# Kernel optimization log

Measured on AMD Instinct MI355X. Metric: run time of the kernel, lower is better.

## Reference

```python
import jax, jax.numpy as jnp
import numpy as np


def setup_inputs() -> dict:
    key = jax.random.key(0)
    ks = jax.random.split(key, 7)
    B, T, D, H, DK, S = 16, 1, 4096, 32, 128, 2048
    return {
        "x": jax.random.normal(ks[0], (B, T, D), dtype=jnp.float32),
        "k_cache": jax.random.normal(ks[1], (B, H, S, DK), dtype=jnp.float32),
        "v_cache": jax.random.normal(ks[2], (B, H, S, DK), dtype=jnp.float32),
        "Wq": jax.random.normal(ks[3], (D, D), dtype=jnp.float32) * (D ** -0.5),
        "Wk": jax.random.normal(ks[4], (D, D), dtype=jnp.float32) * (D ** -0.5),
        "Wv": jax.random.normal(ks[5], (D, D), dtype=jnp.float32) * (D ** -0.5),
        "Wo": jax.random.normal(ks[6], (D, D), dtype=jnp.float32) * (D ** -0.5),
        "start_pos": 2047,
    }


def reference(x, k_cache, v_cache, Wq, Wk, Wv, Wo, start_pos):
    B, T, D = x.shape
    H, DK = k_cache.shape[1], k_cache.shape[3]
    end_pos = start_pos + T

    # QKV projections (nn.Linear with bias=False: y = x @ W.T), split heads -> (B, H, T, DK)
    def proj(W):
        return (x @ W.T).reshape(B, T, H, DK).transpose(0, 2, 1, 3)

    q = proj(Wq)
    k_new = proj(Wk)
    v_new = proj(Wv)

    # Scatter new K/V into the pre-allocated cache at start_pos (static slice)
    k_cache = jax.lax.dynamic_update_slice(k_cache, k_new, (0, 0, start_pos, 0))
    v_cache = jax.lax.dynamic_update_slice(v_cache, v_new, (0, 0, start_pos, 0))

    # Gather cached K/V up to end_pos
    k_all = k_cache[:, :, :end_pos]  # (B, H, end_pos, DK)
    v_all = v_cache[:, :, :end_pos]

    # Scaled dot-product attention with causal mask over cache positions
    scores = jnp.einsum("bhtd,bhsd->bhts", q, k_all) / jnp.sqrt(jnp.float32(DK))
    pos_q = start_pos + jnp.arange(T)          # query absolute positions
    pos_k = jnp.arange(end_pos)                # key absolute positions
    mask = pos_k[None, :] <= pos_q[:, None]    # (T, end_pos)
    scores = jnp.where(mask[None, None], scores, jnp.float32(-1e30))
    attn = jax.nn.softmax(scores, axis=-1)
    out = jnp.einsum("bhts,bhsd->bhtd", attn, v_all)

    # Merge heads and output projection
    out = out.transpose(0, 2, 1, 3).reshape(B, T, D)
    return out @ Wo.T
```

## Files before the change

### kernel.cpp

```cpp
#include <hip/hip_runtime.h>
#include <math.h>

constexpr int B  = 16;
constexpr int H  = 32;
constexpr int S  = 2048;
constexpr int DK = 128;
constexpr int D  = 4096;
constexpr int BH = B * H;

constexpr int NSPLIT = 4;
constexpr int CHUNK  = S / NSPLIT;
constexpr int NREC   = NSPLIT * 4;
constexpr int REC    = 132;

__device__ __forceinline__ float reduce64(float v[64], int lane) {
    #pragma unroll
    for (int s = 0; s < 6; ++s) {
        const int off = 1 << s;
        #pragma unroll
        for (int j = 0; j < (64 >> (s + 1)); ++j) {
            const float lo = v[2 * j], hi = v[2 * j + 1];
            const bool  up = (lane & off) != 0;
            const float mine = up ? hi : lo;
            const float oth  = up ? lo : hi;
            v[j] = mine + __shfl_xor(oth, off, 64);
        }
    }
    return v[0];
}

__global__ __launch_bounds__(256, 3) void proj_qkv_kernel(
    const float* __restrict__ X,
    const float* __restrict__ W0,
    const float* __restrict__ W1,
    const float* __restrict__ W2,
    float* __restrict__ Y0,
    float* __restrict__ Y1,
    float* __restrict__ Y2)
{
    __shared__ float4 xs[2][16][64];

    const int t    = threadIdx.x;
    const int lane = t & 63;
    const int wid  = t >> 6;
    const int tb   = t >> 4;
    const int tf   = t & 15;

    const int c0   = blockIdx.x * 16 + wid * 4;
    const int wsel = c0 >> 12;
    const int n0   = c0 & (D - 1);

    const float* Wp = (wsel == 0) ? W0 : (wsel == 1) ? W1 : W2;
    float*       Yp = (wsel == 0) ? Y0 : (wsel == 1) ? Y1 : Y2;
    const float4* w4 = (const float4*)Wp;
    const float4* x4 = (const float4*)X;

    float acc[64];
    #pragma unroll
    for (int i = 0; i < 64; ++i) acc[i] = 0.f;

    float4 xr[4];
    #pragma unroll
    for (int i = 0; i < 4; ++i) xr[i] = x4[tb * 1024 + tf + 16 * i];
    float4 wv[4];
    #pragma unroll
    for (int c = 0; c < 4; ++c) wv[c] = w4[(size_t)(n0 + c) * 1024 + lane];
    #pragma unroll
    for (int i = 0; i < 4; ++i) xs[0][tb][tf + 16 * i] = xr[i];
    __syncthreads();

    for (int ch = 0; ch < 16; ++ch) {
        float4 xn[4], wn[4];
        const bool more = (ch < 15);
        if (more) {
            #pragma unroll
            for (int i = 0; i < 4; ++i)
                xn[i] = x4[tb * 1024 + (ch + 1) * 64 + tf + 16 * i];
            #pragma unroll
            for (int c = 0; c < 4; ++c)
                wn[c] = w4[(size_t)(n0 + c) * 1024 + (ch + 1) * 64 + lane];
        }
        const int buf = ch & 1;
        #pragma unroll
        for (int b = 0; b < 16; ++b) {
            const float4 xv = xs[buf][b][lane];
            #pragma unroll
            for (int c = 0; c < 4; ++c)
                acc[b * 4 + c] += xv.x * wv[c].x + xv.y * wv[c].y +
                                  xv.z * wv[c].z + xv.w * wv[c].w;
        }
        if (more) {
            #pragma unroll
            for (int i = 0; i < 4; ++i) xs[buf ^ 1][tb][tf + 16 * i] = xn[i];
            __syncthreads();
            #pragma unroll
            for (int c = 0; c < 4; ++c) wv[c] = wn[c];
        }
    }

    const float outv = reduce64(acc, lane);
    Yp[(size_t)(lane >> 2) * D + n0 + (lane & 3)] = outv;
}

__global__ __launch_bounds__(256) void proj_wo_kernel(
    const float* __restrict__ X,
    const float* __restrict__ Wo,
    float* __restrict__ out)
{
    __shared__ float red[4][64];
    const int lane = threadIdx.x & 63;
    const int wid  = threadIdx.x >> 6;
    const int n0   = blockIdx.x * 4;
    const float4* w4 = (const float4*)Wo;
    const float4* x4 = (const float4*)X;

    float acc[64];
    #pragma unroll
    for (int i = 0; i < 64; ++i) acc[i] = 0.f;

    #pragma unroll
    for (int it = 0; it < 4; ++it) {
        const int d4 = wid * 256 + it * 64 + lane;
        float4 wv[4];
        #pragma unroll
        for (int c = 0; c < 4; ++c) wv[c] = w4[(size_t)(n0 + c) * 1024 + d4];
        #pragma unroll
        for (int b = 0; b < 16; ++b) {
            const float4 xv = x4[b * 1024 + d4];
            #pragma unroll
            for (int c = 0; c < 4; ++c)
                acc[b * 4 + c] += xv.x * wv[c].x + xv.y * wv[c].y +
                                  xv.z * wv[c].z + xv.w * wv[c].w;
        }
    }

    const float pv = reduce64(acc, lane);
    red[wid][lane] = pv;
    __syncthreads();
    if (wid == 0) {
        const float tot = red[0][lane] + red[1][lane] + red[2][lane] + red[3][lane];
        out[(size_t)(lane >> 2) * D + n0 + (lane & 3)] = tot;
    }
}

__global__ __launch_bounds__(256) void attn_kernel(
    const float* __restrict__ q,
    const float* __restrict__ k_cache,
    const float* __restrict__ v_cache,
    const float* __restrict__ k_new,
    const float* __restrict__ v_new,
    const int*   __restrict__ start_pos_p,
    float* __restrict__ part)
{
    const int lane  = threadIdx.x & 63;
    const int wid   = threadIdx.x >> 6;
    const int half  = lane >> 5;
    const int hl    = lane & 31;
    const int bh    = blockIdx.x & (BH - 1);
    const int split = blockIdx.x >> 9;

    const int sp    = start_pos_p[0];
    const int s0    = split * CHUNK;
    const int lim   = sp + 1;
    const int s_end = (s0 + CHUNK < lim) ? (s0 + CHUNK) : lim;

    const float qscale = 0.08838834764831845f * 1.4426950408889634f;
    const float shift  = 8.0f * 1.4426950408889634f;
    float4 qv = *(const float4*)(q + (size_t)bh * DK + 4 * hl);
    qv.x *= qscale; qv.y *= qscale; qv.z *= qscale; qv.w *= qscale;

    const float* kbase = k_cache + (size_t)bh * S * DK;
    const float* vbase = v_cache + (size_t)bh * S * DK;
    const float* knew  = k_new + (size_t)bh * DK;
    const float* vnew  = v_new + (size_t)bh * DK;

    float  l = 0.f;
    float4 acc = make_float4(0.f, 0.f, 0.f, 0.f);

    #pragma unroll 2
    for (int s2 = s0 + 2 * wid; s2 < s_end; s2 += 8) {
        const int  pos   = s2 + half;
        const bool valid = pos < s_end;
        const int  cpos  = valid ? pos : (s_end - 1);
        const float* kp = (cpos == sp) ? knew : (kbase + (size_t)cpos * DK);
        const float* vp = (cpos == sp) ? vnew : (vbase + (size_t)cpos * DK);
        const float4 kv = *(const float4*)(kp + 4 * hl);
        const float4 vv = *(const float4*)(vp + 4 * hl);

        float p = kv.x * qv.x + kv.y * qv.y + kv.z * qv.z + kv.w * qv.w;
        p += __shfl_xor(p, 1, 64);
        p += __shfl_xor(p, 2, 64);
        p += __shfl_xor(p, 4, 64);
        p += __shfl_xor(p, 8, 64);
        p += __shfl_xor(p, 16, 64);

        const float ep = valid ? __builtin_amdgcn_exp2f(p - shift) : 0.f;
        l     += ep;
        acc.x += ep * vv.x;
        acc.y += ep * vv.y;
        acc.z += ep * vv.z;
        acc.w += ep * vv.w;
    }

    l     += __shfl_xor(l, 32, 64);
    acc.x += __shfl_xor(acc.x, 32, 64);
    acc.y += __shfl_xor(acc.y, 32, 64);
    acc.z += __shfl_xor(acc.z, 32, 64);
    acc.w += __shfl_xor(acc.w, 32, 64);

    float* rec = part + ((size_t)bh * NREC + split * 4 + wid) * REC;
    if (half == 0) *(float4*)(rec + 4 * hl) = acc;
    if (lane == 0) rec[128] = l;
}

__global__ __launch_bounds__(64) void combine_kernel(
    const float* __restrict__ part,
    float* __restrict__ attn_out)
{
    const int bh   = blockIdx.x;
    const int lane = threadIdx.x;
    const float* base = part + (size_t)bh * NREC * REC;

    float L = 0.f, o0 = 0.f, o1 = 0.f;
    #pragma unroll
    for (int i = 0; i < NREC; ++i) {
        L += base[i * REC + 128];
        const float2 a = *(const float2*)(base + i * REC + 2 * lane);
        o0 += a.x;
        o1 += a.y;
    }
    const float inv = 1.f / L;
    attn_out[(size_t)bh * DK + 2 * lane]     = o0 * inv;
    attn_out[(size_t)bh * DK + 2 * lane + 1] = o1 * inv;
}

extern "C" void kernel_launch(void* const* d_in, const int* in_sizes, int n_in,
                              void* d_out, int out_size, void* d_ws, size_t ws_size,
                              hipStream_t stream)
{
    const float* x       = (const float*)d_in[0];
    const float* k_cache = (const float*)d_in[1];
    const float* v_cache = (const float*)d_in[2];
    const float* Wq      = (const float*)d_in[3];
    const float* Wk      = (const float*)d_in[4];
    const float* Wv      = (const float*)d_in[5];
    const float* Wo      = (const float*)d_in[6];
    const int*   sp      = (const int*)d_in[7];
    float*       out     = (float*)d_out;

    float* ws       = (float*)d_ws;
    float* q        = ws;
    float* k_new    = ws + 65536;
    float* v_new    = ws + 131072;
    float* attn_out = ws + 196608;
    float* part     = ws + 262144;

    proj_qkv_kernel<<<(3 * D) / 16, 256, 0, stream>>>(x, Wq, Wk, Wv, q, k_new, v_new);

    attn_kernel<<<BH * NSPLIT, 256, 0, stream>>>(q, k_cache, v_cache, k_new, v_new,
                                                 sp, part);

    combine_kernel<<<BH, 64, 0, stream>>>(part, attn_out);

    proj_wo_kernel<<<D / 4, 256, 0, stream>>>(attn_out, Wo, out);
}
```

Measured before the change: 307.0 us.

## Unify projection kernels into templated 2-column-per-wave GEMV with single LDS buffer

Replaces the QKV and Wo projection kernels with one templated kernel in which each wave computes 2 output columns instead of 4. The QKV launch uses 512-thread blocks and the Wo launch reuses the same staged-x path. This cuts register pressure (32 accumulators instead of 64) and raises the number of waves in flight for the bandwidth-bound weight streaming. The x tile in LDS drops from double to single buffering, which adds an extra barrier per chunk. The attention loop unroll also goes from 2 to 4.

```diff
diff --git a/kernel.cpp b/kernel.cpp
--- a/kernel.cpp
+++ b/kernel.cpp
@@ -13,12 +13,12 @@
 constexpr int NREC   = NSPLIT * 4;
 constexpr int REC    = 132;
 
-__device__ __forceinline__ float reduce64(float v[64], int lane) {
-    #pragma unroll
-    for (int s = 0; s < 6; ++s) {
+__device__ __forceinline__ float reduce32(float v[32], int lane) {
+    #pragma unroll
+    for (int s = 0; s < 5; ++s) {
         const int off = 1 << s;
         #pragma unroll
-        for (int j = 0; j < (64 >> (s + 1)); ++j) {
+        for (int j = 0; j < (32 >> (s + 1)); ++j) {
             const float lo = v[2 * j], hi = v[2 * j + 1];
             const bool  up = (lane & off) != 0;
             const float mine = up ? hi : lo;
@@ -26,10 +26,11 @@
             v[j] = mine + __shfl_xor(oth, off, 64);
         }
     }
-    return v[0];
-}
-
-__global__ __launch_bounds__(256, 3) void proj_qkv_kernel(
+    return v[0] + __shfl_xor(v[0], 32, 64);
+}
+
+template <int NT>
+__global__ __launch_bounds__(NT, 4) void proj_kernel(
     const float* __restrict__ X,
     const float* __restrict__ W0,
     const float* __restrict__ W1,
@@ -38,15 +39,19 @@
     float* __restrict__ Y1,
     float* __restrict__ Y2)
 {
-    __shared__ float4 xs[2][16][64];
+    constexpr int NW  = NT / 64;
+    constexpr int TPB = NT / 16;
+    constexpr int XPT = 64 / TPB;
+
+    __shared__ float4 xs[16][64];
 
     const int t    = threadIdx.x;
     const int lane = t & 63;
     const int wid  = t >> 6;
-    const int tb   = t >> 4;
-    const int tf   = t & 15;
-
-    const int c0   = blockIdx.x * 16 + wid * 4;
+    const int tb   = t / TPB;
+    const int tf   = t % TPB;
+
+    const int c0   = blockIdx.x * (NW * 2) + wid * 2;
     const int wsel = c0 >> 12;
     const int n0   = c0 & (D - 1);
 
@@ -55,92 +60,56 @@
     const float4* w4 = (const float4*)Wp;
     const float4* x4 = (const float4*)X;
 
-    float acc[64];
-    #pragma unroll
-    for (int i = 0; i < 64; ++i) acc[i] = 0.f;
-
-    float4 xr[4];
-    #pragma unroll
-    for (int i = 0; i < 4; ++i) xr[i] = x4[tb * 1024 + tf + 16 * i];
-    float4 wv[4];
-    #pragma unroll
-    for (int c = 0; c < 4; ++c) wv[c] = w4[(size_t)(n0 + c) * 1024 + lane];
-    #pragma unroll
-    for (int i = 0; i < 4; ++i) xs[0][tb][tf + 16 * i] = xr[i];
+    const size_t r0 = (size_t)(n0 + 0) * 1024;
+    const size_t r1 = (size_t)(n0 + 1) * 1024;
+
+    float acc[32];
+    #pragma unroll
+    for (int i = 0; i < 32; ++i) acc[i] = 0.f;
+
+    float4 xr[XPT];
+    #pragma unroll
+    for (int i = 0; i < XPT; ++i) xr[i] = x4[tb * 1024 + tf + TPB * i];
+    float4 wv0 = w4[r0 + lane];
+    float4 wv1 = w4[r1 + lane];
+    #pragma unroll
+    for (int i = 0; i < XPT; ++i) xs[tb][tf + TPB * i] = xr[i];
     __syncthreads();
 
     for (int ch = 0; ch < 16; ++ch) {
-        float4 xn[4], wn[4];
+        float4 xn[XPT], wn0, wn1;
         const bool more = (ch < 15);
         if (more) {
+            const int kb = (ch + 1) * 64;
             #pragma unroll
-            for (int i = 0; i < 4; ++i)
-                xn[i] = x4[tb * 1024 + (ch + 1) * 64 + tf + 16 * i];
-            #pragma unroll
-            for (int c = 0; c < 4; ++c)
-                wn[c] = w4[(size_t)(n0 + c) * 1024 + (ch + 1) * 64 + lane];
-        }
-        const int buf = ch & 1;
+            for (int i = 0; i < XPT; ++i)
+                xn[i] = x4[tb * 1024 + kb + tf + TPB * i];
+            wn0 = w4[r0 + kb + lane];
+            wn1 = w4[r1 + kb + lane];
+        }
+
         #pragma unroll
         for (int b = 0; b < 16; ++b) {
-            const float4 xv = xs[buf][b][lane];
-            #pragma unroll
-            for (int c = 0; c < 4; ++c)
-                acc[b * 4 + c] += xv.x * wv[c].x + xv.y * wv[c].y +
-                                  xv.z * wv[c].z + xv.w * wv[c].w;
-        }
+            const float4 xv = xs[b][lane];
+            acc[b * 2 + 0] += xv.x * wv0.x + xv.y * wv0.y +
+                              xv.z * wv0.z + xv.w * wv0.w;
+            acc[b * 2 + 1] += xv.x * wv1.x + xv.y * wv1.y +
+                              xv.z * wv1.z + xv.w * wv1.w;
+        }
+
         if (more) {
-            #pragma unroll
-            for (int i = 0; i < 4; ++i) xs[buf ^ 1][tb][tf + 16 * i] = xn[i];
             __syncthreads();
             #pragma unroll
-            for (int c = 0; c < 4; ++c) wv[c] = wn[c];
-        }
-    }
-
-    const float outv = reduce64(acc, lane);
-    Yp[(size_t)(lane >> 2) * D + n0 + (lane & 3)] = outv;
-}
-
-__global__ __launch_bounds__(256) void proj_wo_kernel(
-    const float* __restrict__ X,
-    const float* __restrict__ Wo,
-    float* __restrict__ out)
-{
-    __shared__ float red[4][64];
-    const int lane = threadIdx.x & 63;
-    const int wid  = threadIdx.x >> 6;
-    const int n0   = blockIdx.x * 4;
-    const float4* w4 = (const float4*)Wo;
-    const float4* x4 = (const float4*)X;
-
-    float acc[64];
-    #pragma unroll
-    for (int i = 0; i < 64; ++i) acc[i] = 0.f;
-
-    #pragma unroll
-    for (int it = 0; it < 4; ++it) {
-        const int d4 = wid * 256 + it * 64 + lane;
-        float4 wv[4];
-        #pragma unroll
-        for (int c = 0; c < 4; ++c) wv[c] = w4[(size_t)(n0 + c) * 1024 + d4];
-        #pragma unroll
-        for (int b = 0; b < 16; ++b) {
-            const float4 xv = x4[b * 1024 + d4];
-            #pragma unroll
-            for (int c = 0; c < 4; ++c)
-                acc[b * 4 + c] += xv.x * wv[c].x + xv.y * wv[c].y +
-                                  xv.z * wv[c].z + xv.w * wv[c].w;
-        }
-    }
-
-    const float pv = reduce64(acc, lane);
-    red[wid][lane] = pv;
-    __syncthreads();
-    if (wid == 0) {
-        const float tot = red[0][lane] + red[1][lane] + red[2][lane] + red[3][lane];
-        out[(size_t)(lane >> 2) * D + n0 + (lane & 3)] = tot;
-    }
+            for (int i = 0; i < XPT; ++i) xs[tb][tf + TPB * i] = xn[i];
+            __syncthreads();
+            wv0 = wn0;
+            wv1 = wn1;
+        }
+    }
+
+    const float tot = reduce32(acc, lane);
+    if (lane < 32)
+        Yp[(size_t)(lane >> 1) * D + n0 + (lane & 1)] = tot;
 }
 
 __global__ __launch_bounds__(256) void attn_kernel(
@@ -177,7 +146,7 @@
     float  l = 0.f;
     float4 acc = make_float4(0.f, 0.f, 0.f, 0.f);
 
-    #pragma unroll 2
+    #pragma unroll 4
     for (int s2 = s0 + 2 * wid; s2 < s_end; s2 += 8) {
         const int  pos   = s2 + half;
         const bool valid = pos < s_end;
@@ -255,12 +224,12 @@
     float* attn_out = ws + 196608;
     float* part     = ws + 262144;
 
-    proj_qkv_kernel<<<(3 * D) / 16, 256, 0, stream>>>(x, Wq, Wk, Wv, q, k_new, v_new);
+    proj_kernel<512><<<768, 512, 0, stream>>>(x, Wq, Wk, Wv, q, k_new, v_new);
 
     attn_kernel<<<BH * NSPLIT, 256, 0, stream>>>(q, k_cache, v_cache, k_new, v_new,
                                                  sp, part);
 
     combine_kernel<<<BH, 64, 0, stream>>>(part, attn_out);
 
-    proj_wo_kernel<<<D / 4, 256, 0, stream>>>(attn_out, Wo, out);
-}
+    proj_kernel<256><<<512, 256, 0, stream>>>(attn_out, Wo, Wo, Wo, out, out, out);
+}
```

New measurement: 346.0 us. 12.7% more time.

## Give each attention wave a contiguous key span and batch K then V loads

Applied to the files above, without the earlier changes.

Each wavefront in the attention kernel now handles one contiguous quarter of its chunk instead of interleaved pairs of rows. Within that span it works in tiles of 32 positions: it first issues 16 K loads with their dot products and exponentials, then 16 V loads with their accumulation. The aim is more memory loads in flight per wave and more sequential access per wave over the bandwidth-bound KV cache. The cost is more registers for the ep array, and the fixed tile count relies on SPAN being a multiple of 32.

```diff
diff --git a/kernel.cpp b/kernel.cpp
--- a/kernel.cpp
+++ b/kernel.cpp
@@ -10,6 +10,7 @@
 
 constexpr int NSPLIT = 4;
 constexpr int CHUNK  = S / NSPLIT;
+constexpr int SPAN   = CHUNK / 4;
 constexpr int NREC   = NSPLIT * 4;
 constexpr int REC    = 132;
 
@@ -159,10 +160,11 @@
     const int bh    = blockIdx.x & (BH - 1);
     const int split = blockIdx.x >> 9;
 
-    const int sp    = start_pos_p[0];
-    const int s0    = split * CHUNK;
-    const int lim   = sp + 1;
-    const int s_end = (s0 + CHUNK < lim) ? (s0 + CHUNK) : lim;
+    const int sp     = start_pos_p[0];
+    const int s0     = split * CHUNK;
+    const int lim    = sp + 1;
+    const int s_end  = (s0 + CHUNK < lim) ? (s0 + CHUNK) : lim;
+    const int s_base = s0 + wid * SPAN;
 
     const float qscale = 0.08838834764831845f * 1.4426950408889634f;
     const float shift  = 8.0f * 1.4426950408889634f;
@@ -177,29 +179,45 @@
     float  l = 0.f;
     float4 acc = make_float4(0.f, 0.f, 0.f, 0.f);
 
-    #pragma unroll 2
-    for (int s2 = s0 + 2 * wid; s2 < s_end; s2 += 8) {
-        const int  pos   = s2 + half;
-        const bool valid = pos < s_end;
-        const int  cpos  = valid ? pos : (s_end - 1);
-        const float* kp = (cpos == sp) ? knew : (kbase + (size_t)cpos * DK);
-        const float* vp = (cpos == sp) ? vnew : (vbase + (size_t)cpos * DK);
-        const float4 kv = *(const float4*)(kp + 4 * hl);
-        const float4 vv = *(const float4*)(vp + 4 * hl);
-
-        float p = kv.x * qv.x + kv.y * qv.y + kv.z * qv.z + kv.w * qv.w;
-        p += __shfl_xor(p, 1, 64);
-        p += __shfl_xor(p, 2, 64);
-        p += __shfl_xor(p, 4, 64);
-        p += __shfl_xor(p, 8, 64);
-        p += __shfl_xor(p, 16, 64);
-
-        const float ep = valid ? __builtin_amdgcn_exp2f(p - shift) : 0.f;
-        l     += ep;
-        acc.x += ep * vv.x;
-        acc.y += ep * vv.y;
-        acc.z += ep * vv.z;
-        acc.w += ep * vv.w;
+    for (int tile = 0; tile < SPAN / 32; ++tile) {
+        const int tbase = s_base + tile * 32;
+        float ep[16];
+
+        #pragma unroll
+        for (int i = 0; i < 16; ++i) {
+            const int  pos   = tbase + 2 * i + half;
+            const bool valid = pos < s_end;
+            int cp = valid ? pos : (s_end - 1);
+            cp = (cp < 0) ? 0 : cp;
+            const float* kp = (cp == sp) ? knew : (kbase + (size_t)cp * DK);
+            const float4 kv = *(const float4*)(kp + 4 * hl);
+
+            float p = kv.x * qv.x + kv.y * qv.y + kv.z * qv.z + kv.w * qv.w;
+            p += __shfl_xor(p, 1, 64);
+            p += __shfl_xor(p, 2, 64);
+            p += __shfl_xor(p, 4, 64);
+            p += __shfl_xor(p, 8, 64);
+            p += __shfl_xor(p, 16, 64);
+
+            ep[i] = valid ? __builtin_amdgcn_exp2f(p - shift) : 0.f;
+        }
+
+        #pragma unroll
+        for (int i = 0; i < 16; ++i) {
+            const int  pos   = tbase + 2 * i + half;
+            const bool valid = pos < s_end;
+            int cp = valid ? pos : (s_end - 1);
+            cp = (cp < 0) ? 0 : cp;
+            const float* vp = (cp == sp) ? vnew : (vbase + (size_t)cp * DK);
+            const float4 vv = *(const float4*)(vp + 4 * hl);
+
+            const float e = ep[i];
+            l     += e;
+            acc.x += e * vv.x;
+            acc.y += e * vv.y;
+            acc.z += e * vv.z;
+            acc.w += e * vv.w;
+        }
     }
 
     l     += __shfl_xor(l, 32, 64);
```

New measurement: 328.3 us. +6.9%, slower.

## Drop split-K attention and fuse combine into attention kernel via shared memory

Applied to the files above, without the earlier changes.

Removes the sequence split across four blocks per (batch, head), so each block now processes the whole cache, and replaces the separate combine kernel with an in-block shared-memory reduction. This saves one kernel launch and the global round trip through the partials buffer. In exchange the attention grid shrinks fourfold to 512 blocks, each with a four-times-longer serial loop over 2048 positions, which may leave compute units idle and lower the bandwidth reached while streaming the K/V cache. The loop unroll is raised to help hide memory latency.

```diff
diff --git a/kernel.cpp b/kernel.cpp
--- a/kernel.cpp
+++ b/kernel.cpp
@@ -7,11 +7,6 @@
 constexpr int DK = 128;
 constexpr int D  = 4096;
 constexpr int BH = B * H;
-
-constexpr int NSPLIT = 4;
-constexpr int CHUNK  = S / NSPLIT;
-constexpr int NREC   = NSPLIT * 4;
-constexpr int REC    = 132;
 
 __device__ __forceinline__ float reduce64(float v[64], int lane) {
     #pragma unroll
@@ -150,19 +145,19 @@
     const float* __restrict__ k_new,
     const float* __restrict__ v_new,
     const int*   __restrict__ start_pos_p,
-    float* __restrict__ part)
-{
-    const int lane  = threadIdx.x & 63;
-    const int wid   = threadIdx.x >> 6;
-    const int half  = lane >> 5;
-    const int hl    = lane & 31;
-    const int bh    = blockIdx.x & (BH - 1);
-    const int split = blockIdx.x >> 9;
+    float* __restrict__ attn_out)
+{
+    __shared__ float red[4][132];
+
+    const int lane = threadIdx.x & 63;
+    const int wid  = threadIdx.x >> 6;
+    const int half = lane >> 5;
+    const int hl   = lane & 31;
+    const int bh   = blockIdx.x;
 
     const int sp    = start_pos_p[0];
-    const int s0    = split * CHUNK;
     const int lim   = sp + 1;
-    const int s_end = (s0 + CHUNK < lim) ? (s0 + CHUNK) : lim;
+    const int s_end = (S < lim) ? S : lim;
 
     const float qscale = 0.08838834764831845f * 1.4426950408889634f;
     const float shift  = 8.0f * 1.4426950408889634f;
@@ -177,8 +172,8 @@
     float  l = 0.f;
     float4 acc = make_float4(0.f, 0.f, 0.f, 0.f);
 
-    #pragma unroll 2
-    for (int s2 = s0 + 2 * wid; s2 < s_end; s2 += 8) {
+    #pragma unroll 4
+    for (int s2 = 2 * wid; s2 < s_end; s2 += 8) {
         const int  pos   = s2 + half;
         const bool valid = pos < s_end;
         const int  cpos  = valid ? pos : (s_end - 1);
@@ -208,30 +203,20 @@
     acc.z += __shfl_xor(acc.z, 32, 64);
     acc.w += __shfl_xor(acc.w, 32, 64);
 
-    float* rec = part + ((size_t)bh * NREC + split * 4 + wid) * REC;
-    if (half == 0) *(float4*)(rec + 4 * hl) = acc;
-    if (lane == 0) rec[128] = l;
-}
-
-__global__ __launch_bounds__(64) void combine_kernel(
-    const float* __restrict__ part,
-    float* __restrict__ attn_out)
-{
-    const int bh   = blockIdx.x;
-    const int lane = threadIdx.x;
-    const float* base = part + (size_t)bh * NREC * REC;
-
-    float L = 0.f, o0 = 0.f, o1 = 0.f;
-    #pragma unroll
-    for (int i = 0; i < NREC; ++i) {
-        L += base[i * REC + 128];
-        const float2 a = *(const float2*)(base + i * REC + 2 * lane);
-        o0 += a.x;
-        o1 += a.y;
-    }
-    const float inv = 1.f / L;
-    attn_out[(size_t)bh * DK + 2 * lane]     = o0 * inv;
-    attn_out[(size_t)bh * DK + 2 * lane + 1] = o1 * inv;
+    if (half == 0) *(float4*)(&red[wid][4 * hl]) = acc;
+    if (lane == 0) red[wid][128] = l;
+    __syncthreads();
+
+    if (wid == 0) {
+        const float L  = red[0][128] + red[1][128] + red[2][128] + red[3][128];
+        const float o0 = red[0][2 * lane]     + red[1][2 * lane] +
+                         red[2][2 * lane]     + red[3][2 * lane];
+        const float o1 = red[0][2 * lane + 1] + red[1][2 * lane + 1] +
+                         red[2][2 * lane + 1] + red[3][2 * lane + 1];
+        const float inv = 1.f / L;
+        attn_out[(size_t)bh * DK + 2 * lane]     = o0 * inv;
+        attn_out[(size_t)bh * DK + 2 * lane + 1] = o1 * inv;
+    }
 }
 
 extern "C" void kernel_launch(void* const* d_in, const int* in_sizes, int n_in,
@@ -253,14 +238,11 @@
     float* k_new    = ws + 65536;
     float* v_new    = ws + 131072;
     float* attn_out = ws + 196608;
-    float* part     = ws + 262144;
 
     proj_qkv_kernel<<<(3 * D) / 16, 256, 0, stream>>>(x, Wq, Wk, Wv, q, k_new, v_new);
 
-    attn_kernel<<<BH * NSPLIT, 256, 0, stream>>>(q, k_cache, v_cache, k_new, v_new,
-                                                 sp, part);
-
-    combine_kernel<<<BH, 64, 0, stream>>>(part, attn_out);
+    attn_kernel<<<BH, 256, 0, stream>>>(q, k_cache, v_cache, k_new, v_new,
+                                        sp, attn_out);
 
     proj_wo_kernel<<<D / 4, 256, 0, stream>>>(attn_out, Wo, out);
 }
```

Result: slower. 329.8 us (+7.4%).
